# Kernel optimization log

Measured on AMD Instinct MI355X. Metric: run time of the kernel, lower is better.

Reference implementation:

```python
import jax, jax.numpy as jnp
import numpy as np

SCALE = 10  # scaling_factor
ETA = 1.0   # init arg eta
EPS = 1e-20


def setup_inputs() -> dict:
    key = jax.random.key(0)
    k1, k2, k3 = jax.random.split(key, 3)
    B, H, W = 32, 1280, 1280
    h, w = H // SCALE, W // SCALE
    output = jax.random.uniform(k1, (B, 1, H, W), dtype=jnp.float32)
    target = jax.random.uniform(k2, (B, 1, H, W), dtype=jnp.float32)
    inp = jax.random.uniform(k3, (B, 1, h, w), dtype=jnp.float32)
    return {"output": output, "target": target, "inp": inp}


def _box_downsample(x):
    # scipy valid convolve2d with ones(10,10)/100 then [::10,::10] strided slice
    # == non-overlapping 10x10 average pooling (H, W divisible by 10).
    B, H, W = x.shape
    return x.reshape(B, H // SCALE, SCALE, W // SCALE, SCALE).mean(axis=(2, 4))


def reference(output, target, inp):
    # MSE term: conv output is computed from detached numpy in the original,
    # so no gradient flows through the pooling path -> stop_gradient.
    pooled = jax.lax.stop_gradient(_box_downsample(output[:, 0]))  # [B, h, w]
    mse = jnp.mean(ETA * (inp[:, 0] - pooled) ** 2)
    # BCE-style term with exact-zero replacement (matches x[x==0]=1e-20)
    om = jnp.where(output == 0, EPS, output)
    oc_raw = 1.0 - output
    oc = jnp.where(oc_raw == 0, EPS, oc_raw)
    bce = -jnp.mean(target * jnp.log(om) + (1.0 - target) * jnp.log(oc))
    loss = mse + bce
    return jnp.full((1, 1), loss)  # original returns a (1,1) tensor
```

## Files before the change

### kernel.cpp

```cpp
#include <hip/hip_runtime.h>


#define BATCH 32
#define HH 1280
#define WW 1280
#define PH 128
#define PW 128
#define SC 10

static constexpr float EPSV = 1e-20f;
static constexpr float INV_NB = 1.0f / (float)(BATCH * HH * WW);
static constexpr float INV_NM = 1.0f / (float)(BATCH * PH * PW);

__global__ __launch_bounds__(256) void srloss_kernel(
    const float* __restrict__ output,
    const float* __restrict__ target,
    const float* __restrict__ inp,
    float* __restrict__ out)
{
    __shared__ float psum[PW];
    __shared__ float red[4];

    const int t = threadIdx.x;
    const int band = blockIdx.x;
    const int b = band / PH;
    const int pr = band % PH;

    if (t < PW) psum[t] = 0.0f;
    __syncthreads();

    const size_t base = ((size_t)b * HH + (size_t)pr * SC) * WW;
    const float4* __restrict__ o4p = (const float4*)(output + base);
    const float4* __restrict__ t4p = (const float4*)(target + base);

    float bce_acc = 0.0f;
    const int NV = (SC * WW) / 4;
    for (int c = t; c < NV; c += 256) {
        const float4 o4 = o4p[c];
        const float4 t4 = t4p[c];
        float o[4]  = {o4.x, o4.y, o4.z, o4.w};
        float tg[4] = {t4.x, t4.y, t4.z, t4.w};
        float s = 0.0f;
        #pragma unroll
        for (int j = 0; j < 4; ++j) {
            float om  = (o[j] == 0.0f) ? EPSV : o[j];
            float ocr = 1.0f - o[j];
            float oc  = (ocr == 0.0f) ? EPSV : ocr;
            s += tg[j] * __logf(om) + (1.0f - tg[j]) * __logf(oc);
        }
        bce_acc += s;

        const int col0 = (4 * c) % WW;
        const int p0 = col0 / SC;
        const int r = col0 % SC;
        if (r == 8) {
            atomicAdd(&psum[p0],     o[0] + o[1]);
            atomicAdd(&psum[p0 + 1], o[2] + o[3]);
        } else {
            atomicAdd(&psum[p0], (o[0] + o[1]) + (o[2] + o[3]));
        }
    }
    __syncthreads();

    float mse_acc = 0.0f;
    if (t < PW) {
        const float pooled = psum[t] * (1.0f / (float)(SC * SC));
        const float iv = inp[(size_t)band * PW + t];
        const float d = iv - pooled;
        mse_acc = d * d;
    }

    float contrib = (-INV_NB) * bce_acc + INV_NM * mse_acc;

    #pragma unroll
    for (int off = 32; off > 0; off >>= 1)
        contrib += __shfl_down(contrib, off, 64);
    const int wave = t >> 6;
    if ((t & 63) == 0) red[wave] = contrib;
    __syncthreads();
    if (t == 0) {
        atomicAdd(out, (red[0] + red[1]) + (red[2] + red[3]));
    }
}

extern "C" void kernel_launch(void* const* d_in, const int* in_sizes, int n_in,
                              void* d_out, int out_size, void* d_ws, size_t ws_size,
                              hipStream_t stream) {
    const float* output = (const float*)d_in[0];
    const float* target = (const float*)d_in[1];
    const float* inp    = (const float*)d_in[2];
    float* out = (float*)d_out;

    hipMemsetAsync(out, 0, sizeof(float), stream);

    srloss_kernel<<<BATCH * PH, 256, 0, stream>>>(output, target, inp, out);
}
```

Baseline: 431.5 us.

## Use 640-thread blocks with hoisted loads and per-thread pooling accumulation

Raises block size to 640 so each thread handles a fixed column across five rows, issuing all ten float4 loads up front before computing. Because each thread's column is constant, pooling sums accumulate in registers and need only one or two shared atomics per thread instead of one per vector. This targets poor memory-level parallelism and LDS atomic contention, at the cost of higher register use per thread.

```diff
diff --git a/kernel.cpp b/kernel.cpp
--- a/kernel.cpp
+++ b/kernel.cpp
@@ -7,24 +7,27 @@
 #define PH 128
 #define PW 128
 #define SC 10
+#define NT 640
+#define NV ((SC * WW) / 4)
+#define KITER (NV / NT)
 
 static constexpr float EPSV = 1e-20f;
 static constexpr float INV_NB = 1.0f / (float)(BATCH * HH * WW);
 static constexpr float INV_NM = 1.0f / (float)(BATCH * PH * PW);
 
-__global__ __launch_bounds__(256) void srloss_kernel(
+__global__ __launch_bounds__(NT) void srloss_kernel(
     const float* __restrict__ output,
     const float* __restrict__ target,
     const float* __restrict__ inp,
     float* __restrict__ out)
 {
     __shared__ float psum[PW];
-    __shared__ float red[4];
+    __shared__ float red[NT / 64];
 
     const int t = threadIdx.x;
     const int band = blockIdx.x;
-    const int b = band / PH;
-    const int pr = band % PH;
+    const int b = band >> 7;
+    const int pr = band & 127;
 
     if (t < PW) psum[t] = 0.0f;
     __syncthreads();
@@ -33,32 +36,36 @@
     const float4* __restrict__ o4p = (const float4*)(output + base);
     const float4* __restrict__ t4p = (const float4*)(target + base);
 
+    float4 ov[KITER], tv[KITER];
+    #pragma unroll
+    for (int k = 0; k < KITER; ++k) ov[k] = o4p[t + NT * k];
+    #pragma unroll
+    for (int k = 0; k < KITER; ++k) tv[k] = t4p[t + NT * k];
+
     float bce_acc = 0.0f;
-    const int NV = (SC * WW) / 4;
-    for (int c = t; c < NV; c += 256) {
-        const float4 o4 = o4p[c];
-        const float4 t4 = t4p[c];
-        float o[4]  = {o4.x, o4.y, o4.z, o4.w};
-        float tg[4] = {t4.x, t4.y, t4.z, t4.w};
-        float s = 0.0f;
+    float s0 = 0.0f, s1 = 0.0f;
+    #pragma unroll
+    for (int k = 0; k < KITER; ++k) {
+        const float o[4]  = {ov[k].x, ov[k].y, ov[k].z, ov[k].w};
+        const float tg[4] = {tv[k].x, tv[k].y, tv[k].z, tv[k].w};
         #pragma unroll
         for (int j = 0; j < 4; ++j) {
-            float om  = (o[j] == 0.0f) ? EPSV : o[j];
-            float ocr = 1.0f - o[j];
-            float oc  = (ocr == 0.0f) ? EPSV : ocr;
-            s += tg[j] * __logf(om) + (1.0f - tg[j]) * __logf(oc);
+            const float om  = (o[j] == 0.0f) ? EPSV : o[j];
+            const float ocr = 1.0f - o[j];
+            const float oc  = (ocr == 0.0f) ? EPSV : ocr;
+            bce_acc += tg[j] * __logf(om) + (1.0f - tg[j]) * __logf(oc);
         }
-        bce_acc += s;
+        s0 += o[0] + o[1];
+        s1 += o[2] + o[3];
+    }
 
-        const int col0 = (4 * c) % WW;
-        const int p0 = col0 / SC;
-        const int r = col0 % SC;
-        if (r == 8) {
-            atomicAdd(&psum[p0],     o[0] + o[1]);
-            atomicAdd(&psum[p0 + 1], o[2] + o[3]);
-        } else {
-            atomicAdd(&psum[p0], (o[0] + o[1]) + (o[2] + o[3]));
-        }
+    const int col0 = 4 * (t % 320);
+    const int p0 = col0 / SC;
+    if ((col0 % SC) == 8) {
+        atomicAdd(&psum[p0],     s0);
+        atomicAdd(&psum[p0 + 1], s1);
+    } else {
+        atomicAdd(&psum[p0], s0 + s1);
     }
     __syncthreads();
 
@@ -75,11 +82,13 @@
     #pragma unroll
     for (int off = 32; off > 0; off >>= 1)
         contrib += __shfl_down(contrib, off, 64);
-    const int wave = t >> 6;
-    if ((t & 63) == 0) red[wave] = contrib;
+    if ((t & 63) == 0) red[t >> 6] = contrib;
     __syncthreads();
     if (t == 0) {
-        atomicAdd(out, (red[0] + red[1]) + (red[2] + red[3]));
+        float s = 0.0f;
+        #pragma unroll
+        for (int w = 0; w < NT / 64; ++w) s += red[w];
+        atomicAdd(out, s);
     }
 }
 
@@ -93,5 +102,5 @@
 
     hipMemsetAsync(out, 0, sizeof(float), stream);
 
-    srloss_kernel<<<BATCH * PH, 256, 0, stream>>>(output, target, inp, out);
+    srloss_kernel<<<BATCH * PH, NT, 0, stream>>>(output, target, inp, out);
 }
```

New measurement: 413.8 us. 1.04x faster.
